# Performance work log

Measured on AMD Instinct MI355X. Metric: run time of the kernel, lower is better.

The kernel has to match this reference:

```python
import jax, jax.numpy as jnp
from jax import lax
import numpy as np

B, DIM, H, W = 1, 48, 192, 192
HEADS, K, DIL = 2, 7, 3
HD = DIM // HEADS
HID = int(DIM * 2.66)  # 127 (Restormer GEGLU hidden)
EPS = 1e-5


def _window_starts(L, Kk, D):
    # NATTEN window-start rule: keep phase i % D, shift window inside bounds.
    s = np.zeros(L, dtype=np.int32)
    for i in range(L):
        if D <= 1:
            st = max(i - Kk // 2, 0)
            if i + Kk // 2 >= L:
                st = L - Kk
        else:
            st = i - (Kk // 2) * D
            if st < 0:
                st = i % D
            elif i + (Kk // 2) * D >= L:
                imodd = i % D
                a = (L // D) * D
                b = L - a
                if imodd < b:
                    st = L - b + imodd - 2 * (Kk // 2) * D
                else:
                    st = a + imodd - Kk * D
        s[i] = st
    return s


def _nbr_tables(L, Kk, D):
    st = _window_starts(L, Kk, D)
    idx = st[:, None] + np.arange(Kk)[None, :] * D          # [L, K] absolute neighbor idx
    pb = (st - np.arange(L)) // D                            # signed offset of window start (in dilation units)
    pb = pb[:, None] + (Kk - 1) + np.arange(Kk)[None, :]     # [L, K] rpb index in [0, 2K-2]
    return jnp.asarray(idx), jnp.asarray(pb)

IH, PBH = _nbr_tables(H, K, DIL)
IW, PBW = _nbr_tables(W, K, DIL)


def layernorm(x, w, b):  # channel LN on NCHW (WithBias, biased var)
    mu = x.mean(1, keepdims=True)
    var = ((x - mu) ** 2).mean(1, keepdims=True)
    return (x - mu) / jnp.sqrt(var + EPS) * w[None, :, None, None] + b[None, :, None, None]


def na2d(x, qkv_w, qkv_b, rpb, proj_w, proj_b):
    # x: NCHW -> BHWC
    t = x.transpose(0, 2, 3, 1)
    qkv = t @ qkv_w.T + qkv_b                                # [B,H,W,3*DIM]
    qkv = qkv.reshape(B, H, W, 3, HEADS, HD)
    q, k, v = qkv[:, :, :, 0], qkv[:, :, :, 1], qkv[:, :, :, 2]
    q = q * (HD ** -0.5)
    # gather dilated 7x7 neighborhoods: [B, H, K, W, K, heads, hd]
    kn = k[:, IH[:, :, None, None], IW[None, None, :, :]]
    vn = v[:, IH[:, :, None, None], IW[None, None, :, :]]
    attn = jnp.einsum('bijnc,bixjync->bijnxy', q, kn)        # [B,H,W,heads,K,K]
    bias = rpb[:, PBH][:, :, :, PBW]                         # [heads,H,K,W,K]
    attn = attn + bias.transpose(1, 3, 0, 2, 4)
    attn = jax.nn.softmax(attn.reshape(B, H, W, HEADS, K * K), axis=-1)
    attn = attn.reshape(B, H, W, HEADS, K, K)
    out = jnp.einsum('bijnxy,bixjync->bijnc', attn, vn).reshape(B, H, W, DIM)
    out = out @ proj_w.T + proj_b
    return out.transpose(0, 3, 1, 2)


def chan_mod(x, eca_w):  # ECA-style gate: GAP -> 1D conv over channels -> sigmoid
    p = x.mean((2, 3))                                       # [B,C]
    y = lax.conv_general_dilated(p[:, None, :], eca_w[None, None, :], (1,), [(3, 3)],
                                 dimension_numbers=('NCH', 'OIH', 'NCH'))[:, 0, :]
    return jax.nn.sigmoid(y)[:, :, None, None]


def ffn(x, w_in, w_dw, w_out):  # conv-GEGLU
    t = jnp.einsum('bchw,oc->bohw', x, w_in)                 # 1x1: DIM -> 2*HID
    t = lax.conv_general_dilated(t, w_dw, (1, 1), [(1, 1), (1, 1)],
                                 feature_group_count=2 * HID,
                                 dimension_numbers=('NCHW', 'OIHW', 'NCHW'))
    x1, x2 = t[:, :HID], t[:, HID:]
    g = jax.nn.gelu(x1, approximate=False) * x2
    return jnp.einsum('bchw,oc->bohw', g, w_out)             # 1x1: HID -> DIM


def setup_inputs() -> dict:
    key = jax.random.key(0)
    ks = jax.random.split(key, 10)
    d = {
        'x': jax.random.normal(ks[0], (B, DIM, H, W), jnp.float32),
        'ln1_w': jnp.ones((DIM,), jnp.float32),
        'ln1_b': jnp.zeros((DIM,), jnp.float32),
        'qkv_w': jax.random.normal(ks[1], (3 * DIM, DIM), jnp.float32) * 0.05,
        'qkv_b': jnp.zeros((3 * DIM,), jnp.float32),
        'rpb': jax.random.normal(ks[2], (HEADS, 2 * K - 1, 2 * K - 1), jnp.float32) * 0.02,
        'proj_w': jax.random.normal(ks[3], (DIM, DIM), jnp.float32) * 0.05,
        'proj_b': jnp.zeros((DIM,), jnp.float32),
        'eca_w': jax.random.normal(ks[4], (7,), jnp.float32) * 0.1,
        'ln2_w': jnp.ones((DIM,), jnp.float32),
        'ln2_b': jnp.zeros((DIM,), jnp.float32),
        'w_in': jax.random.normal(ks[5], (2 * HID, DIM), jnp.float32) * 0.05,
        'w_dw': jax.random.normal(ks[6], (2 * HID, 1, 3, 3), jnp.float32) * 0.05,
        'w_out': jax.random.normal(ks[7], (DIM, HID), jnp.float32) * 0.05,
    }
    return d


def reference(x, ln1_w, ln1_b, qkv_w, qkv_b, rpb, proj_w, proj_b, eca_w,
              ln2_w, ln2_b, w_in, w_dw, w_out):
    xn1 = layernorm(x, ln1_w, ln1_b)
    x = x + na2d(xn1, qkv_w, qkv_b, rpb, proj_w, proj_b) * chan_mod(xn1, eca_w)
    x = x + ffn(layernorm(x, ln2_w, ln2_b), w_in, w_dw, w_out)
    return x
```

## Files before the change

### kernel.cpp

```cpp
#include <hip/hip_runtime.h>
#include <hip/hip_bf16.h>
#include <math.h>

#define HW_ (192*192)
#define Wd 192
#define HIDc 127
#define NBLK1 (HW_/64)

#define O_LN1W 0
#define O_QKVW 96
#define O_QKVB 7008
#define O_RPB  7152
#define O_PROJW 7490
#define O_PROJB 9794
#define O_ECA  9842
#define O_LN2W 9849
#define O_WIN  9945
#define O_WDW  22137
#define O_WOUT 24423
#define WTS_LEN 30519

typedef unsigned short ushort_t;

__device__ __forceinline__ float b2f(__hip_bfloat16 v){ return __bfloat162float(v); }
__device__ __forceinline__ float u2f(ushort_t h){ return __uint_as_float(((unsigned)h)<<16); }
__device__ __forceinline__ ushort_t f2u(float f){
    __hip_bfloat16 h = __float2bfloat16(f);
    union { __hip_bfloat16 b; ushort_t u; } c; c.b = h; return c.u;
}
__device__ __forceinline__ void up2(unsigned u, float& a, float& b){
    a = __uint_as_float(u << 16);
    b = __uint_as_float(u & 0xffff0000u);
}

__device__ __forceinline__ int wstart(int i){
    if (i < 9) return i % 3;
    if (i >= 183) return 171 + (i % 3);
    return i - 9;
}

__device__ __forceinline__ float dot48bf(const uint4* wr, const float* xr){
    float acc = 0.f;
    #pragma unroll
    for (int c8 = 0; c8 < 6; c8++){
        uint4 u = wr[c8];
        float f0,f1,f2,f3,f4,f5,f6,f7;
        up2(u.x,f0,f1); up2(u.y,f2,f3); up2(u.z,f4,f5); up2(u.w,f6,f7);
        acc += f0*xr[8*c8]   + f1*xr[8*c8+1] + f2*xr[8*c8+2] + f3*xr[8*c8+3]
             + f4*xr[8*c8+4] + f5*xr[8*c8+5] + f6*xr[8*c8+6] + f7*xr[8*c8+7];
    }
    return acc;
}

__global__ void convert_kernel(
    const void* p0, const void* p1, const void* p2, const void* p3,
    const void* p4, const void* p5, const void* p6, const void* p7,
    const void* p8, const void* p9, const void* p10, const void* p11,
    const void* p12, const ushort_t* __restrict__ xu, int* __restrict__ mode_out,
    float* __restrict__ wts, ushort_t* __restrict__ qkvbf, ushort_t* __restrict__ woutTbf,
    ushort_t* __restrict__ winbf, ushort_t* __restrict__ projbf)
{
    __shared__ int sbad;
    if (threadIdx.x == 0) sbad = 0;
    __syncthreads();
    {
        unsigned u = xu[2*threadIdx.x];
        float f = __uint_as_float(u << 16);
        if (!(fabsf(f) < 100.f)) atomicAdd(&sbad, 1);
    }
    __syncthreads();
    const int md = (sbad > 16) ? 1 : 0;
    if (blockIdx.x == 0 && threadIdx.x == 0) mode_out[0] = md;

    const void* ps[13] = {p0,p1,p2,p3,p4,p5,p6,p7,p8,p9,p10,p11,p12};
    const int sz[13]  = {48,48,6912,144,338,2304,48,7,48,48,12192,2286,6096};
    const int off[13] = {O_LN1W,48,O_QKVW,O_QKVB,O_RPB,O_PROJW,O_PROJB,O_ECA,
                         O_LN2W,9897,O_WIN,O_WDW,O_WOUT};
    int b = blockIdx.x;
    if (b >= 13){
        if (b == 13){
            if (md){
                const float* s = (const float*)p2;
                for (int i = threadIdx.x; i < 6912; i += 256) qkvbf[i] = f2u(s[i]);
            } else {
                const ushort_t* s = (const ushort_t*)p2;
                for (int i = threadIdx.x; i < 6912; i += 256) qkvbf[i] = s[i];
            }
        } else if (b == 14){
            if (md){
                const float* s = (const float*)p12;
                for (int i = threadIdx.x; i < 6096; i += 256){
                    int c = i / 48, o = i - c*48;
                    woutTbf[i] = f2u(s[o*127 + c]);
                }
            } else {
                const ushort_t* s = (const ushort_t*)p12;
                for (int i = threadIdx.x; i < 6096; i += 256){
                    int c = i / 48, o = i - c*48;
                    woutTbf[i] = s[o*127 + c];
                }
            }
        } else if (b == 15){
            if (md){
                const float* s = (const float*)p10;
                for (int i = threadIdx.x; i < 12192; i += 256) winbf[i] = f2u(s[i]);
            } else {
                const ushort_t* s = (const ushort_t*)p10;
                for (int i = threadIdx.x; i < 12192; i += 256) winbf[i] = s[i];
            }
        } else {
            if (md){
                const float* s = (const float*)p5;
                for (int i = threadIdx.x; i < 2304; i += 256) projbf[i] = f2u(s[i]);
            } else {
                const ushort_t* s = (const ushort_t*)p5;
                for (int i = threadIdx.x; i < 2304; i += 256) projbf[i] = s[i];
            }
        }
        return;
    }
    int n = sz[b];
    float* dst = wts + off[b];
    if (md){
        const float* s = (const float*)ps[b];
        for (int i = threadIdx.x; i < n; i += 256) dst[i] = s[i];
    } else {
        const __hip_bfloat16* s = (const __hip_bfloat16*)ps[b];
        for (int i = threadIdx.x; i < n; i += 256) dst[i] = b2f(s[i]);
    }
}

__global__ __launch_bounds__(384) void ln1qkv_kernel(
    const void* __restrict__ x, const int* __restrict__ mode,
    const float* __restrict__ wts, const ushort_t* __restrict__ qkvbf,
    ushort_t* __restrict__ q, ushort_t* __restrict__ k, ushort_t* __restrict__ v,
    float* __restrict__ chpart)
{
    __shared__ float sx[64*49];

    const int tid  = threadIdx.x;
    const int px_l = tid & 63;
    const int r6   = __builtin_amdgcn_readfirstlane(tid >> 6);
    const int p0   = blockIdx.x * 64;
    const int p    = p0 + px_l;

    if (mode[0]){
        const float* xf = (const float*)x;
        for (int idx = tid; idx < 64*48; idx += 384){
            int c = idx >> 6, pl = idx & 63;
            sx[pl*49 + c] = xf[c*HW_ + p0 + pl];
        }
    } else {
        const __hip_bfloat16* xb = (const __hip_bfloat16*)x;
        for (int idx = tid; idx < 64*48; idx += 384){
            int c = idx >> 6, pl = idx & 63;
            sx[pl*49 + c] = b2f(xb[c*HW_ + p0 + pl]);
        }
    }
    __syncthreads();

    float xr[48];
    float mu = 0.f;
    #pragma unroll
    for (int c = 0; c < 48; c++){ xr[c] = sx[px_l*49 + c]; mu += xr[c]; }
    mu *= (1.f/48.f);
    float var = 0.f;
    #pragma unroll
    for (int c = 0; c < 48; c++){ float d = xr[c]-mu; var += d*d; }
    var *= (1.f/48.f);
    float rs = rsqrtf(var + 1e-5f);
    #pragma unroll
    for (int c = 0; c < 48; c++)
        xr[c] = (xr[c]-mu)*rs*wts[O_LN1W + c] + wts[O_LN1W + 48 + c];

    if (tid < 64){
        #pragma unroll
        for (int c = 0; c < 48; c++){
            float s = xr[c];
            s += __shfl_xor(s, 1);  s += __shfl_xor(s, 2);  s += __shfl_xor(s, 4);
            s += __shfl_xor(s, 8);  s += __shfl_xor(s, 16); s += __shfl_xor(s, 32);
            if (tid == 0) chpart[blockIdx.x*48 + c] = s;
        }
    }

    const int rbase = r6 * 24;
    const float scale = (r6 < 2) ? 0.20412414523193154f : 1.0f;
    float ov[24];
    #pragma unroll 4
    for (int ro = 0; ro < 24; ro++){
        int r = rbase + ro;
        float acc = wts[O_QKVB + r]
                  + dot48bf((const uint4*)(qkvbf + r*48), xr);
        ov[ro] = acc * scale;
    }

    unsigned int pk[12];
    #pragma unroll
    for (int d = 0; d < 12; d++)
        pk[d] = (unsigned)f2u(ov[2*d]) | ((unsigned)f2u(ov[2*d+1]) << 16);
    ushort_t* tp = (r6 >> 1) == 0 ? q : ((r6 >> 1) == 1 ? k : v);
    uint4* dst4 = (uint4*)(tp + (size_t)p*48 + (r6 & 1)*24);
    dst4[0] = make_uint4(pk[0], pk[1], pk[2],  pk[3]);
    dst4[1] = make_uint4(pk[4], pk[5], pk[6],  pk[7]);
    dst4[2] = make_uint4(pk[8], pk[9], pk[10], pk[11]);
}

__global__ __launch_bounds__(256) void gatefuse_kernel(
    const float* __restrict__ chpart, const float* __restrict__ wts,
    float* __restrict__ gate)
{
    __shared__ float sm[48];
    const int t = threadIdx.x;
    if (t < 192){
        const int ch = t >> 2, qq = t & 3;
        float acc = 0.f;
        #pragma unroll 4
        for (int b = qq; b < NBLK1; b += 4)
            acc += chpart[b*48 + ch];
        acc += __shfl_xor(acc, 1);
        acc += __shfl_xor(acc, 2);
        if (qq == 0) sm[ch] = acc * (1.f / (float)HW_);
    }
    __syncthreads();
    if (t < 48){
        float a = 0.f;
        for (int kk = 0; kk < 7; kk++){
            int cc = t + kk - 3;
            if (cc >= 0 && cc < 48) a += wts[O_ECA + kk] * sm[cc];
        }
        gate[t] = 1.f / (1.f + expf(-a));
    }
}

__global__ __launch_bounds__(256) void attnproj_kernel(
    const ushort_t* __restrict__ q, const ushort_t* __restrict__ k,
    const ushort_t* __restrict__ v, const float* __restrict__ wts,
    const ushort_t* __restrict__ projbf, const float* __restrict__ gate,
    const void* __restrict__ x, const int* __restrict__ mode,
    float* __restrict__ x2)
{
    __shared__ float srpb[338];
    __shared__ float sa[64*49];

    const int tid = threadIdx.x;
    for (int i0 = tid; i0 < 338; i0 += 256) srpb[i0] = wts[O_RPB + i0];
    __syncthreads();

    const int parity = tid & 1;
    const int head   = (tid >> 1) & 1;
    const int px_l   = tid >> 2;
    const int px     = blockIdx.x * 64 + px_l;
    const int i = px / Wd, j = px % Wd;
    const int sti = wstart(i), stj = wstart(j);
    const int pbi = (sti - i) / 3 + 6;
    const int pbj = (stj - j) / 3 + 6;
    const int choff = head * 24;
    const float* rpb = srpb + head*169;

    float qr[24];
    {
        const uint4* qp = (const uint4*)(q + (size_t)px*48 + choff);
        uint4 q0 = qp[0], q1 = qp[1], q2 = qp[2];
        up2(q0.x,qr[0],qr[1]);   up2(q0.y,qr[2],qr[3]);
        up2(q0.z,qr[4],qr[5]);   up2(q0.w,qr[6],qr[7]);
        up2(q1.x,qr[8],qr[9]);   up2(q1.y,qr[10],qr[11]);
        up2(q1.z,qr[12],qr[13]); up2(q1.w,qr[14],qr[15]);
        up2(q2.x,qr[16],qr[17]); up2(q2.y,qr[18],qr[19]);
        up2(q2.z,qr[20],qr[21]); up2(q2.w,qr[22],qr[23]);
    }

    float m = -1e30f, s = 0.f;
    float acc[24];
    #pragma unroll
    for (int c = 0; c < 24; c++) acc[c] = 0.f;

    #pragma unroll 5
    for (int t = 0; t < 25; t++){
        int n = 2*t + parity;
        const bool inval = (n > 48);
        if (inval) n = 48;
        int xx = (n * 147) >> 10;
        int yy = n - 7*xx;
        int ii = sti + 3*xx, jj = stj + 3*yy;
        const size_t nb = (size_t)(ii*Wd + jj)*48 + choff;
        const uint4* kp = (const uint4*)(k + nb);
        const uint4* vp = (const uint4*)(v + nb);
        uint4 K0 = kp[0], K1 = kp[1], K2 = kp[2];
        uint4 V0 = vp[0], V1 = vp[1], V2 = vp[2];
        float a, b;
        float d = 0.f;
        up2(K0.x,a,b); d += qr[0]*a  + qr[1]*b;
        up2(K0.y,a,b); d += qr[2]*a  + qr[3]*b;
        up2(K0.z,a,b); d += qr[4]*a  + qr[5]*b;
        up2(K0.w,a,b); d += qr[6]*a  + qr[7]*b;
        up2(K1.x,a,b); d += qr[8]*a  + qr[9]*b;
        up2(K1.y,a,b); d += qr[10]*a + qr[11]*b;
        up2(K1.z,a,b); d += qr[12]*a + qr[13]*b;
        up2(K1.w,a,b); d += qr[14]*a + qr[15]*b;
        up2(K2.x,a,b); d += qr[16]*a + qr[17]*b;
        up2(K2.y,a,b); d += qr[18]*a + qr[19]*b;
        up2(K2.z,a,b); d += qr[20]*a + qr[21]*b;
        up2(K2.w,a,b); d += qr[22]*a + qr[23]*b;
        float sc = d + rpb[(pbi+xx)*13 + (pbj+yy)];
        if (inval) sc = -1e30f;
        float mn = fmaxf(m, sc);
        float corr = __expf(m - mn);
        float p = __expf(sc - mn);
        s = s*corr + p;
        m = mn;
        up2(V0.x,a,b); acc[0] =acc[0] *corr + p*a; acc[1] =acc[1] *corr + p*b;
        up2(V0.y,a,b); acc[2] =acc[2] *corr + p*a; acc[3] =acc[3] *corr + p*b;
        up2(V0.z,a,b); acc[4] =acc[4] *corr + p*a; acc[5] =acc[5] *corr + p*b;
        up2(V0.w,a,b); acc[6] =acc[6] *corr + p*a; acc[7] =acc[7] *corr + p*b;
        up2(V1.x,a,b); acc[8] =acc[8] *corr + p*a; acc[9] =acc[9] *corr + p*b;
        up2(V1.y,a,b); acc[10]=acc[10]*corr + p*a; acc[11]=acc[11]*corr + p*b;
        up2(V1.z,a,b); acc[12]=acc[12]*corr + p*a; acc[13]=acc[13]*corr + p*b;
        up2(V1.w,a,b); acc[14]=acc[14]*corr + p*a; acc[15]=acc[15]*corr + p*b;
        up2(V2.x,a,b); acc[16]=acc[16]*corr + p*a; acc[17]=acc[17]*corr + p*b;
        up2(V2.y,a,b); acc[18]=acc[18]*corr + p*a; acc[19]=acc[19]*corr + p*b;
        up2(V2.z,a,b); acc[20]=acc[20]*corr + p*a; acc[21]=acc[21]*corr + p*b;
        up2(V2.w,a,b); acc[22]=acc[22]*corr + p*a; acc[23]=acc[23]*corr + p*b;
    }

    {
        float mo = __shfl_xor(m, 1);
        float so = __shfl_xor(s, 1);
        float mn = fmaxf(m, mo);
        float ca = __expf(m - mn), cb = __expf(mo - mn);
        s = s*ca + so*cb;
        #pragma unroll
        for (int c = 0; c < 24; c++)
            acc[c] = acc[c]*ca + __shfl_xor(acc[c], 1)*cb;
    }
    const float inv = 1.f / s;
    {
        float* dst = sa + px_l*49 + choff + parity*12;
        if (parity == 0){
            #pragma unroll
            for (int c = 0; c < 12; c++) dst[c] = acc[c] * inv;
        } else {
            #pragma unroll
            for (int c = 0; c < 12; c++) dst[c] = acc[12 + c] * inv;
        }
    }
    __syncthreads();

    const int px_l2 = tid & 63;
    const int og    = __builtin_amdgcn_readfirstlane(tid >> 6);
    const int px2   = blockIdx.x * 64 + px_l2;

    float ar[48];
    #pragma unroll
    for (int c = 0; c < 48; c++) ar[c] = sa[px_l2*49 + c];

    const float* xf = (const float*)x;
    const __hip_bfloat16* xb = (const __hip_bfloat16*)x;
    const int md = mode[0];
    const int ob = og * 12;
    #pragma unroll 2
    for (int oo = 0; oo < 12; oo++){
        int o = ob + oo;
        float accp = wts[O_PROJB + o]
                   + dot48bf((const uint4*)(projbf + o*48), ar);
        float res = md ? xf[o*HW_ + px2] : b2f(xb[o*HW_ + px2]);
        x2[o*HW_ + px2] = res + accp * gate[o];
    }
}

__global__ __launch_bounds__(256) void pw1_kernel(
    const float* __restrict__ x2, const float* __restrict__ wts,
    const ushort_t* __restrict__ winbf, ushort_t* __restrict__ t)
{
    const int tid  = threadIdx.x;
    const int px_l = tid & 63;
    const int og   = __builtin_amdgcn_readfirstlane(tid >> 6);
    const int px   = blockIdx.x * 64 + px_l;

    float xr[48];
    float mu = 0.f;
    #pragma unroll
    for (int c = 0; c < 48; c++){ xr[c] = x2[c*HW_ + px]; mu += xr[c]; }
    mu *= (1.f/48.f);
    float var = 0.f;
    #pragma unroll
    for (int c = 0; c < 48; c++){ float d = xr[c]-mu; var += d*d; }
    var *= (1.f/48.f);
    float rs = rsqrtf(var + 1e-5f);
    #pragma unroll
    for (int c = 0; c < 48; c++)
        xr[c] = (xr[c]-mu)*rs*wts[O_LN2W + c] + wts[O_LN2W + 48 + c];

    const int base = blockIdx.y * 128 + og * 32;
    for (int t2 = 0; t2 < 32; t2 += 2){
        int o0 = base + t2;
        if (o0 >= 254) break;
        const uint4* wA = (const uint4*)(winbf + o0*48);
        const uint4* wB = (const uint4*)(winbf + min(o0+1,253)*48);
        float accA = 0.f, accB = 0.f;
        #pragma unroll
        for (int c8 = 0; c8 < 6; c8++){
            uint4 ua = wA[c8];
            uint4 ub = wB[c8];
            float a0,a1,a2,a3,a4,a5,a6,a7, b0,b1,b2,b3,b4,b5,b6,b7;
            up2(ua.x,a0,a1); up2(ua.y,a2,a3); up2(ua.z,a4,a5); up2(ua.w,a6,a7);
            up2(ub.x,b0,b1); up2(ub.y,b2,b3); up2(ub.z,b4,b5); up2(ub.w,b6,b7);
            accA += a0*xr[8*c8]   + a1*xr[8*c8+1] + a2*xr[8*c8+2] + a3*xr[8*c8+3]
                  + a4*xr[8*c8+4] + a5*xr[8*c8+5] + a6*xr[8*c8+6] + a7*xr[8*c8+7];
            accB += b0*xr[8*c8]   + b1*xr[8*c8+1] + b2*xr[8*c8+2] + b3*xr[8*c8+3]
                  + b4*xr[8*c8+4] + b5*xr[8*c8+5] + b6*xr[8*c8+6] + b7*xr[8*c8+7];
        }
        t[(size_t)o0*HW_ + px] = f2u(accA);
        if (o0+1 < 254) t[(size_t)(o0+1)*HW_ + px] = f2u(accB);
    }
}

__global__ __launch_bounds__(256) void dw_kernel(
    const ushort_t* __restrict__ t, const float* __restrict__ wts,
    ushort_t* __restrict__ g)
{
    const int ch = blockIdx.y;
    const int pp = (blockIdx.x * 256 + threadIdx.x) * 4;
    const int i  = pp / Wd, j = pp % Wd;
    float w1[9], w2[9];
    #pragma unroll
    for (int s2 = 0; s2 < 9; s2++){
        w1[s2] = wts[O_WDW + ch*9 + s2];
        w2[s2] = wts[O_WDW + (ch+HIDc)*9 + s2];
    }
    const ushort_t* t1 = t + (size_t)ch * HW_;
    const ushort_t* t2 = t + (size_t)(ch+HIDc) * HW_;
    float a10=0.f,a11=0.f,a12=0.f,a13=0.f;
    float a20=0.f,a21=0.f,a22=0.f,a23=0.f;
    #pragma unroll
    for (int di = 0; di < 3; di++){
        int ii = i + di - 1;
        if (ii < 0 || ii >= 192) continue;
        int base = ii*Wd + j;
        float wa = w1[di*3], wb = w1[di*3+1], wc = w1[di*3+2];
        {
            uint2 mm = *(const uint2*)(t1 + base);
            float c0,c1,c2,c3; up2(mm.x,c0,c1); up2(mm.y,c2,c3);
            float cm = (j > 0)     ? u2f(t1[base-1]) : 0.f;
            float cp = (j+4 < Wd)  ? u2f(t1[base+4]) : 0.f;
            a10 += wa*cm + wb*c0 + wc*c1;
            a11 += wa*c0 + wb*c1 + wc*c2;
            a12 += wa*c1 + wb*c2 + wc*c3;
            a13 += wa*c2 + wb*c3 + wc*cp;
        }
        wa = w2[di*3]; wb = w2[di*3+1]; wc = w2[di*3+2];
        {
            uint2 mm = *(const uint2*)(t2 + base);
            float c0,c1,c2,c3; up2(mm.x,c0,c1); up2(mm.y,c2,c3);
            float cm = (j > 0)     ? u2f(t2[base-1]) : 0.f;
            float cp = (j+4 < Wd)  ? u2f(t2[base+4]) : 0.f;
            a20 += wa*cm + wb*c0 + wc*c1;
            a21 += wa*c0 + wb*c1 + wc*c2;
            a22 += wa*c1 + wb*c2 + wc*c3;
            a23 += wa*c2 + wb*c3 + wc*cp;
        }
    }
    const float RS2 = 0.70710678118654752f;
    float g0 = a10 * 0.5f * (1.f + erff(a10 * RS2)) * a20;
    float g1 = a11 * 0.5f * (1.f + erff(a11 * RS2)) * a21;
    float g2 = a12 * 0.5f * (1.f + erff(a12 * RS2)) * a22;
    float g3 = a13 * 0.5f * (1.f + erff(a13 * RS2)) * a23;
    uint2 pk;
    pk.x = (unsigned)f2u(g0) | ((unsigned)f2u(g1) << 16);
    pk.y = (unsigned)f2u(g2) | ((unsigned)f2u(g3) << 16);
    *(uint2*)(g + (size_t)ch*HW_ + pp) = pk;
}

__global__ __launch_bounds__(128) void pw2_kernel(
    const ushort_t* __restrict__ g, const ushort_t* __restrict__ woutTbf,
    const float* __restrict__ x2, void* __restrict__ outv,
    const int* __restrict__ mode)
{
    const int ob = blockIdx.y * 12;
    const int p  = blockIdx.x * 128 + threadIdx.x;
    float acc[12];
    #pragma unroll
    for (int o = 0; o < 12; o++) acc[o] = 0.f;
    #pragma unroll 4
    for (int c = 0; c < 127; c++){
        float gv = u2f(g[(size_t)c*HW_ + p]);
        const unsigned* wr = (const unsigned*)(woutTbf + c*48 + ob);
        #pragma unroll
        for (int d = 0; d < 6; d++){
            float w0, w1;
            up2(wr[d], w0, w1);
            acc[2*d]   += w0*gv;
            acc[2*d+1] += w1*gv;
        }
    }
    if (mode[0]){
        float* out = (float*)outv;
        #pragma unroll
        for (int o = 0; o < 12; o++){
            int oc = ob + o;
            out[(size_t)oc*HW_ + p] = x2[(size_t)oc*HW_ + p] + acc[o];
        }
    } else {
        __hip_bfloat16* out = (__hip_bfloat16*)outv;
        #pragma unroll
        for (int o = 0; o < 12; o++){
            int oc = ob + o;
            out[(size_t)oc*HW_ + p] =
                __float2bfloat16(x2[(size_t)oc*HW_ + p] + acc[o]);
        }
    }
}

extern "C" void kernel_launch(void* const* d_in, const int* in_sizes, int n_in,
                              void* d_out, int out_size, void* d_ws, size_t ws_size,
                              hipStream_t stream)
{
    (void)in_sizes; (void)n_in; (void)out_size;

    char* ws = (char*)d_ws;
    ushort_t* q    = (ushort_t*)(ws);
    ushort_t* k    = (ushort_t*)(ws + 3538944);
    ushort_t* v    = (ushort_t*)(ws + 7077888);
    ushort_t* t    = (ushort_t*)(ws);
    float*    x2   = (float*)   (ws + 18726912);
    ushort_t* g    = (ushort_t*)(ws + 25804800);
    float*    gate = (float*)   (ws + 35168448);
    int*      mode = (int*)     (ws + 35168640);
    float*    wts  = (float*)   (ws + 35168656);
    float*    chpart=(float*)   (ws + 35168656 + (size_t)WTS_LEN*4);
    float*    msum = chpart + (size_t)NBLK1*48;
    ushort_t* qkvbf= (ushort_t*)(msum + 48);
    ushort_t* woutTbf = qkvbf + 6912;
    ushort_t* winbf   = woutTbf + 6096;
    ushort_t* projbf  = winbf + 12192;

    size_t need = 35168656 + (size_t)WTS_LEN*4 + (size_t)NBLK1*48*4 + 48*4
                + (6912 + 6096 + 12192 + 2304)*2;
    if (ws_size < need) return;

    convert_kernel<<<17, 256, 0, stream>>>(
        d_in[1], d_in[2], d_in[3], d_in[4], d_in[5], d_in[6], d_in[7],
        d_in[8], d_in[9], d_in[10], d_in[11], d_in[12], d_in[13],
        (const ushort_t*)d_in[0], mode, wts, qkvbf, woutTbf, winbf, projbf);

    ln1qkv_kernel<<<dim3(NBLK1), 384, 0, stream>>>(d_in[0], mode, wts, qkvbf,
                                                   q, k, v, chpart);
    gatefuse_kernel<<<1, 256, 0, stream>>>(chpart, wts, gate);
    attnproj_kernel<<<dim3(HW_/64), 256, 0, stream>>>(q, k, v, wts, projbf, gate,
                                                      d_in[0], mode, x2);
    pw1_kernel<<<dim3(HW_/64, 2), 256, 0, stream>>>(x2, wts, winbf, t);
    dw_kernel<<<dim3(HW_/1024, 127), 256, 0, stream>>>(t, wts, g);
    pw2_kernel<<<dim3(HW_/128, 4), 128, 0, stream>>>(g, woutTbf, x2, d_out, mode);
}
```

Baseline: 239.6 us.

## Fuse LN2 and FFN input projection into attention kernel, use fp16 QKV

Merges the pw1 kernel (LayerNorm2 plus the 48-to-254 input projection) into the attention/projection kernel, reusing the residual values held in shared memory so x2 is not re-read from global memory and one launch goes away. Q, K and V are now stored as fp16 instead of bf16. The online softmax is replaced by a plain exp with the score clamped at 80, which removes the running-max correction from the inner loop. The costs are more work per block (each 64-thread group now computes 64 output channels) and a new workspace layout. The missing max subtraction relies on scores staying small, and fp16 narrows the representable range.

After: 237.6 us. Within noise of the previous version (-0.8%).

```diff
diff --git a/kernel.cpp b/kernel.cpp
--- a/kernel.cpp
+++ b/kernel.cpp
@@ -21,6 +21,7 @@
 #define WTS_LEN 30519
 
 typedef unsigned short ushort_t;
+typedef _Float16 half2_t __attribute__((ext_vector_type(2)));
 
 __device__ __forceinline__ float b2f(__hip_bfloat16 v){ return __bfloat162float(v); }
 __device__ __forceinline__ float u2f(ushort_t h){ return __uint_as_float(((unsigned)h)<<16); }
@@ -31,6 +32,16 @@
 __device__ __forceinline__ void up2(unsigned u, float& a, float& b){
     a = __uint_as_float(u << 16);
     b = __uint_as_float(u & 0xffff0000u);
+}
+__device__ __forceinline__ unsigned pkh2(float a, float b){
+    half2_t h; h[0] = (_Float16)a; h[1] = (_Float16)b;
+    union { half2_t h; unsigned u; } c; c.h = h; return c.u;
+}
+__device__ __forceinline__ half2_t u2h2(unsigned u){
+    union { unsigned u; half2_t h; } c; c.u = u; return c.h;
+}
+__device__ __forceinline__ float dot2h(half2_t a, half2_t b, float c){
+    return c + (float)a[0]*(float)b[0] + (float)a[1]*(float)b[1];
 }
 
 __device__ __forceinline__ int wstart(int i){
@@ -197,7 +208,7 @@
     unsigned int pk[12];
     #pragma unroll
     for (int d = 0; d < 12; d++)
-        pk[d] = (unsigned)f2u(ov[2*d]) | ((unsigned)f2u(ov[2*d+1]) << 16);
+        pk[d] = pkh2(ov[2*d], ov[2*d+1]);
     ushort_t* tp = (r6 >> 1) == 0 ? q : ((r6 >> 1) == 1 ? k : v);
     uint4* dst4 = (uint4*)(tp + (size_t)p*48 + (r6 & 1)*24);
     dst4[0] = make_uint4(pk[0], pk[1], pk[2],  pk[3]);
@@ -232,12 +243,13 @@
     }
 }
 
-__global__ __launch_bounds__(256) void attnproj_kernel(
+__global__ __launch_bounds__(256) void attnfuse_kernel(
     const ushort_t* __restrict__ q, const ushort_t* __restrict__ k,
     const ushort_t* __restrict__ v, const float* __restrict__ wts,
     const ushort_t* __restrict__ projbf, const float* __restrict__ gate,
     const void* __restrict__ x, const int* __restrict__ mode,
-    float* __restrict__ x2)
+    float* __restrict__ x2, const ushort_t* __restrict__ winbf,
+    ushort_t* __restrict__ tout)
 {
     __shared__ float srpb[338];
     __shared__ float sa[64*49];
@@ -257,26 +269,23 @@
     const int choff = head * 24;
     const float* rpb = srpb + head*169;
 
-    float qr[24];
+    half2_t qh[12];
     {
         const uint4* qp = (const uint4*)(q + (size_t)px*48 + choff);
         uint4 q0 = qp[0], q1 = qp[1], q2 = qp[2];
-        up2(q0.x,qr[0],qr[1]);   up2(q0.y,qr[2],qr[3]);
-        up2(q0.z,qr[4],qr[5]);   up2(q0.w,qr[6],qr[7]);
-        up2(q1.x,qr[8],qr[9]);   up2(q1.y,qr[10],qr[11]);
-        up2(q1.z,qr[12],qr[13]); up2(q1.w,qr[14],qr[15]);
-        up2(q2.x,qr[16],qr[17]); up2(q2.y,qr[18],qr[19]);
-        up2(q2.z,qr[20],qr[21]); up2(q2.w,qr[22],qr[23]);
-    }
-
-    float m = -1e30f, s = 0.f;
+        qh[0]=u2h2(q0.x); qh[1]=u2h2(q0.y); qh[2] =u2h2(q0.z); qh[3] =u2h2(q0.w);
+        qh[4]=u2h2(q1.x); qh[5]=u2h2(q1.y); qh[6] =u2h2(q1.z); qh[7] =u2h2(q1.w);
+        qh[8]=u2h2(q2.x); qh[9]=u2h2(q2.y); qh[10]=u2h2(q2.z); qh[11]=u2h2(q2.w);
+    }
+
+    float s = 0.f;
     float acc[24];
     #pragma unroll
     for (int c = 0; c < 24; c++) acc[c] = 0.f;
 
     #pragma unroll 5
-    for (int t = 0; t < 25; t++){
-        int n = 2*t + parity;
+    for (int tt = 0; tt < 25; tt++){
+        int n = 2*tt + parity;
         const bool inval = (n > 48);
         if (inval) n = 48;
         int xx = (n * 147) >> 10;
@@ -287,61 +296,52 @@
         const uint4* vp = (const uint4*)(v + nb);
         uint4 K0 = kp[0], K1 = kp[1], K2 = kp[2];
         uint4 V0 = vp[0], V1 = vp[1], V2 = vp[2];
-        float a, b;
         float d = 0.f;
-        up2(K0.x,a,b); d += qr[0]*a  + qr[1]*b;
-        up2(K0.y,a,b); d += qr[2]*a  + qr[3]*b;
-        up2(K0.z,a,b); d += qr[4]*a  + qr[5]*b;
-        up2(K0.w,a,b); d += qr[6]*a  + qr[7]*b;
-        up2(K1.x,a,b); d += qr[8]*a  + qr[9]*b;
-        up2(K1.y,a,b); d += qr[10]*a + qr[11]*b;
-        up2(K1.z,a,b); d += qr[12]*a + qr[13]*b;
-        up2(K1.w,a,b); d += qr[14]*a + qr[15]*b;
-        up2(K2.x,a,b); d += qr[16]*a + qr[17]*b;
-        up2(K2.y,a,b); d += qr[18]*a + qr[19]*b;
-        up2(K2.z,a,b); d += qr[20]*a + qr[21]*b;
-        up2(K2.w,a,b); d += qr[22]*a + qr[23]*b;
+        d = dot2h(u2h2(K0.x), qh[0],  d);
+        d = dot2h(u2h2(K0.y), qh[1],  d);
+        d = dot2h(u2h2(K0.z), qh[2],  d);
+        d = dot2h(u2h2(K0.w), qh[3],  d);
+        d = dot2h(u2h2(K1.x), qh[4],  d);
+        d = dot2h(u2h2(K1.y), qh[5],  d);
+        d = dot2h(u2h2(K1.z), qh[6],  d);
+        d = dot2h(u2h2(K1.w), qh[7],  d);
+        d = dot2h(u2h2(K2.x), qh[8],  d);
+        d = dot2h(u2h2(K2.y), qh[9],  d);
+        d = dot2h(u2h2(K2.z), qh[10], d);
+        d = dot2h(u2h2(K2.w), qh[11], d);
         float sc = d + rpb[(pbi+xx)*13 + (pbj+yy)];
+        sc = fminf(sc, 80.f);
         if (inval) sc = -1e30f;
-        float mn = fmaxf(m, sc);
-        float corr = __expf(m - mn);
-        float p = __expf(sc - mn);
-        s = s*corr + p;
-        m = mn;
-        up2(V0.x,a,b); acc[0] =acc[0] *corr + p*a; acc[1] =acc[1] *corr + p*b;
-        up2(V0.y,a,b); acc[2] =acc[2] *corr + p*a; acc[3] =acc[3] *corr + p*b;
-        up2(V0.z,a,b); acc[4] =acc[4] *corr + p*a; acc[5] =acc[5] *corr + p*b;
-        up2(V0.w,a,b); acc[6] =acc[6] *corr + p*a; acc[7] =acc[7] *corr + p*b;
-        up2(V1.x,a,b); acc[8] =acc[8] *corr + p*a; acc[9] =acc[9] *corr + p*b;
-        up2(V1.y,a,b); acc[10]=acc[10]*corr + p*a; acc[11]=acc[11]*corr + p*b;
-        up2(V1.z,a,b); acc[12]=acc[12]*corr + p*a; acc[13]=acc[13]*corr + p*b;
-        up2(V1.w,a,b); acc[14]=acc[14]*corr + p*a; acc[15]=acc[15]*corr + p*b;
-        up2(V2.x,a,b); acc[16]=acc[16]*corr + p*a; acc[17]=acc[17]*corr + p*b;
-        up2(V2.y,a,b); acc[18]=acc[18]*corr + p*a; acc[19]=acc[19]*corr + p*b;
-        up2(V2.z,a,b); acc[20]=acc[20]*corr + p*a; acc[21]=acc[21]*corr + p*b;
-        up2(V2.w,a,b); acc[22]=acc[22]*corr + p*a; acc[23]=acc[23]*corr + p*b;
-    }
-
-    {
-        float mo = __shfl_xor(m, 1);
-        float so = __shfl_xor(s, 1);
-        float mn = fmaxf(m, mo);
-        float ca = __expf(m - mn), cb = __expf(mo - mn);
-        s = s*ca + so*cb;
-        #pragma unroll
-        for (int c = 0; c < 24; c++)
-            acc[c] = acc[c]*ca + __shfl_xor(acc[c], 1)*cb;
-    }
+        float p = __expf(sc);
+        s += p;
+        half2_t vv;
+        vv=u2h2(V0.x); acc[0] +=p*(float)vv[0]; acc[1] +=p*(float)vv[1];
+        vv=u2h2(V0.y); acc[2] +=p*(float)vv[0]; acc[3] +=p*(float)vv[1];
+        vv=u2h2(V0.z); acc[4] +=p*(float)vv[0]; acc[5] +=p*(float)vv[1];
+        vv=u2h2(V0.w); acc[6] +=p*(float)vv[0]; acc[7] +=p*(float)vv[1];
+        vv=u2h2(V1.x); acc[8] +=p*(float)vv[0]; acc[9] +=p*(float)vv[1];
+        vv=u2h2(V1.y); acc[10]+=p*(float)vv[0]; acc[11]+=p*(float)vv[1];
+        vv=u2h2(V1.z); acc[12]+=p*(float)vv[0]; acc[13]+=p*(float)vv[1];
+        vv=u2h2(V1.w); acc[14]+=p*(float)vv[0]; acc[15]+=p*(float)vv[1];
+        vv=u2h2(V2.x); acc[16]+=p*(float)vv[0]; acc[17]+=p*(float)vv[1];
+        vv=u2h2(V2.y); acc[18]+=p*(float)vv[0]; acc[19]+=p*(float)vv[1];
+        vv=u2h2(V2.z); acc[20]+=p*(float)vv[0]; acc[21]+=p*(float)vv[1];
+        vv=u2h2(V2.w); acc[22]+=p*(float)vv[0]; acc[23]+=p*(float)vv[1];
+    }
+
+    s += __shfl_xor(s, 1);
     const float inv = 1.f / s;
+    float mg[12];
+    #pragma unroll
+    for (int c = 0; c < 12; c++){
+        float mine   = parity ? acc[12+c] : acc[c];
+        float theirs = parity ? acc[c]    : acc[12+c];
+        mg[c] = (mine + __shfl_xor(theirs, 1)) * inv;
+    }
     {
         float* dst = sa + px_l*49 + choff + parity*12;
-        if (parity == 0){
-            #pragma unroll
-            for (int c = 0; c < 12; c++) dst[c] = acc[c] * inv;
-        } else {
-            #pragma unroll
-            for (int c = 0; c < 12; c++) dst[c] = acc[12 + c] * inv;
-        }
+        #pragma unroll
+        for (int c = 0; c < 12; c++) dst[c] = mg[c];
     }
     __syncthreads();
 
@@ -352,6 +352,7 @@
     float ar[48];
     #pragma unroll
     for (int c = 0; c < 48; c++) ar[c] = sa[px_l2*49 + c];
+    __syncthreads();
 
     const float* xf = (const float*)x;
     const __hip_bfloat16* xb = (const __hip_bfloat16*)x;
@@ -363,35 +364,28 @@
         float accp = wts[O_PROJB + o]
                    + dot48bf((const uint4*)(projbf + o*48), ar);
         float res = md ? xf[o*HW_ + px2] : b2f(xb[o*HW_ + px2]);
-        x2[o*HW_ + px2] = res + accp * gate[o];
-    }
-}
-
-__global__ __launch_bounds__(256) void pw1_kernel(
-    const float* __restrict__ x2, const float* __restrict__ wts,
-    const ushort_t* __restrict__ winbf, ushort_t* __restrict__ t)
-{
-    const int tid  = threadIdx.x;
-    const int px_l = tid & 63;
-    const int og   = __builtin_amdgcn_readfirstlane(tid >> 6);
-    const int px   = blockIdx.x * 64 + px_l;
+        float xv = res + accp * gate[o];
+        x2[o*HW_ + px2] = xv;
+        sa[px_l2*49 + o] = xv;
+    }
+    __syncthreads();
 
     float xr[48];
     float mu = 0.f;
     #pragma unroll
-    for (int c = 0; c < 48; c++){ xr[c] = x2[c*HW_ + px]; mu += xr[c]; }
+    for (int c = 0; c < 48; c++){ xr[c] = sa[px_l2*49 + c]; mu += xr[c]; }
     mu *= (1.f/48.f);
     float var = 0.f;
     #pragma unroll
-    for (int c = 0; c < 48; c++){ float d = xr[c]-mu; var += d*d; }
+    for (int c = 0; c < 48; c++){ float dd = xr[c]-mu; var += dd*dd; }
     var *= (1.f/48.f);
     float rs = rsqrtf(var + 1e-5f);
     #pragma unroll
     for (int c = 0; c < 48; c++)
         xr[c] = (xr[c]-mu)*rs*wts[O_LN2W + c] + wts[O_LN2W + 48 + c];
 
-    const int base = blockIdx.y * 128 + og * 32;
-    for (int t2 = 0; t2 < 32; t2 += 2){
+    const int base = og * 64;
+    for (int t2 = 0; t2 < 64; t2 += 2){
         int o0 = base + t2;
         if (o0 >= 254) break;
         const uint4* wA = (const uint4*)(winbf + o0*48);
@@ -409,8 +403,8 @@
             accB += b0*xr[8*c8]   + b1*xr[8*c8+1] + b2*xr[8*c8+2] + b3*xr[8*c8+3]
                   + b4*xr[8*c8+4] + b5*xr[8*c8+5] + b6*xr[8*c8+6] + b7*xr[8*c8+7];
         }
-        t[(size_t)o0*HW_ + px] = f2u(accA);
-        if (o0+1 < 254) t[(size_t)(o0+1)*HW_ + px] = f2u(accB);
+        tout[(size_t)o0*HW_ + px2] = f2u(accA);
+        if (o0+1 < 254) tout[(size_t)(o0+1)*HW_ + px2] = f2u(accB);
     }
 }
 
@@ -520,21 +514,19 @@
     ushort_t* q    = (ushort_t*)(ws);
     ushort_t* k    = (ushort_t*)(ws + 3538944);
     ushort_t* v    = (ushort_t*)(ws + 7077888);
-    ushort_t* t    = (ushort_t*)(ws);
-    float*    x2   = (float*)   (ws + 18726912);
-    ushort_t* g    = (ushort_t*)(ws + 25804800);
-    float*    gate = (float*)   (ws + 35168448);
-    int*      mode = (int*)     (ws + 35168640);
-    float*    wts  = (float*)   (ws + 35168656);
-    float*    chpart=(float*)   (ws + 35168656 + (size_t)WTS_LEN*4);
-    float*    msum = chpart + (size_t)NBLK1*48;
-    ushort_t* qkvbf= (ushort_t*)(msum + 48);
-    ushort_t* woutTbf = qkvbf + 6912;
-    ushort_t* winbf   = woutTbf + 6096;
-    ushort_t* projbf  = winbf + 12192;
-
-    size_t need = 35168656 + (size_t)WTS_LEN*4 + (size_t)NBLK1*48*4 + 48*4
-                + (6912 + 6096 + 12192 + 2304)*2;
+    float*    x2   = (float*)   (ws + 10616832);
+    ushort_t* t    = (ushort_t*)(ws + 17694720);
+    ushort_t* g    = (ushort_t*)(ws);
+    float*    gate = (float*)   (ws + 36421632);
+    int*      mode = (int*)     (ws + 36421824);
+    float*    wts  = (float*)   (ws + 36421840);
+    float*    chpart=(float*)   (ws + 36543920);
+    ushort_t* qkvbf   = (ushort_t*)(ws + 36654512);
+    ushort_t* woutTbf = (ushort_t*)(ws + 36668336);
+    ushort_t* winbf   = (ushort_t*)(ws + 36680528);
+    ushort_t* projbf  = (ushort_t*)(ws + 36704912);
+
+    size_t need = 36709520;
     if (ws_size < need) return;
 
     convert_kernel<<<17, 256, 0, stream>>>(
@@ -545,9 +537,8 @@
     ln1qkv_kernel<<<dim3(NBLK1), 384, 0, stream>>>(d_in[0], mode, wts, qkvbf,
                                                    q, k, v, chpart);
     gatefuse_kernel<<<1, 256, 0, stream>>>(chpart, wts, gate);
-    attnproj_kernel<<<dim3(HW_/64), 256, 0, stream>>>(q, k, v, wts, projbf, gate,
-                                                      d_in[0], mode, x2);
-    pw1_kernel<<<dim3(HW_/64, 2), 256, 0, stream>>>(x2, wts, winbf, t);
+    attnfuse_kernel<<<dim3(HW_/64), 256, 0, stream>>>(q, k, v, wts, projbf, gate,
+                                                      d_in[0], mode, x2, winbf, t);
     dw_kernel<<<dim3(HW_/1024, 127), 256, 0, stream>>>(t, wts, g);
     pw2_kernel<<<dim3(HW_/128, 4), 128, 0, stream>>>(g, woutTbf, x2, d_out, mode);
 }
```
